# Performance work log

Hardware: AMD Instinct MI355X
Metric: run time of the kernel (lower is better)

The kernel has to match this reference:

```python
import jax, jax.numpy as jnp
import numpy as np

SCALE = 1.0 / np.sqrt(128.0)  # 1/sqrt(head_size)
NEG = -1000000000.0


def setup_inputs() -> dict:
    key = jax.random.key(0)
    k1, k2, k3, k4 = jax.random.split(key, 4)
    B, H, S, D = 2, 16, 2048, 128
    q = jax.random.normal(k1, (B, H, S, D), dtype=jnp.float32)
    k = jax.random.normal(k2, (B, H, S, D), dtype=jnp.float32)
    v = jax.random.normal(k3, (B, H, S, D), dtype=jnp.float32)
    mask = jax.random.randint(k4, (B, S), 0, 2, dtype=jnp.int32)
    return {"q": q, "k": k, "v": v, "mask": mask}


def reference(q, k, v, mask):
    # scores: [B, H, Sq, Sk]
    scores = jnp.einsum("bhqd,bhkd->bhqk", q, k) * SCALE
    m = mask[:, None, None, :]  # [B,1,1,Sk], broadcast over heads and queries
    scores = jnp.where(m == 0, NEG, scores)
    weights = jax.nn.softmax(scores, axis=-1)
    out = jnp.einsum("bhqk,bhkd->bhqd", weights, v)
    return out
```

## Files before the change

### kernel.cpp

```cpp
#include <hip/hip_runtime.h>
#include <hip/hip_bf16.h>

typedef __attribute__((ext_vector_type(8))) short short8;
typedef __attribute__((ext_vector_type(4))) short short4v;
typedef __attribute__((ext_vector_type(4))) float floatx4;

#define NB 2
#define NH 16
#define NBH 32
#define SS 2048
#define DD 128
#define BQ 256
#define BK 32
#define KTILES (SS / BK)
#define SCALE 0.08838834764831845f
#define LOG2E 1.4426950408889634f
#define MAXB 12.0f
#define MASKED_BIAS -100000.0f

#if __has_builtin(__builtin_amdgcn_mfma_f32_16x16x16bf16_1k)
#define MFMA16(a, b, c) __builtin_amdgcn_mfma_f32_16x16x16bf16_1k(a, b, c, 0, 0, 0)
#elif __has_builtin(__builtin_amdgcn_mfma_f32_16x16x16_bf16)
#define MFMA16(a, b, c) __builtin_amdgcn_mfma_f32_16x16x16_bf16(a, b, c, 0, 0, 0)
#else
__device__ __forceinline__ floatx4 mfma16_asm(short4v a, short4v b, floatx4 c) {
  asm volatile("v_mfma_f32_16x16x16_bf16 %0, %1, %2, %0" : "+v"(c) : "v"(a), "v"(b));
  return c;
}
#define MFMA16(a, b, c) mfma16_asm(a, b, c)
#endif

__device__ __forceinline__ short f2bf(float f) {
  union { float f; unsigned u; } x; x.f = f;
  return (short)((x.u + 0x7FFFu + ((x.u >> 16) & 1u)) >> 16);
}

__device__ __forceinline__ short4v pack4(float a, float b, float c, float d) {
  union { __hip_bfloat162 h2[2]; short4v v; } u;
  u.h2[0] = __float22bfloat162_rn(make_float2(a, b));
  u.h2[1] = __float22bfloat162_rn(make_float2(c, d));
  return u.v;
}

__device__ __forceinline__ void gload_lds16(const short* g, short* l) {
  __builtin_amdgcn_global_load_lds(
      (const __attribute__((address_space(1))) void*)(g),
      (__attribute__((address_space(3))) void*)(l), 16, 0, 0);
}

__global__ __launch_bounds__(256) void prep_kernel(const float* __restrict__ k,
                                                   const float* __restrict__ v,
                                                   short* __restrict__ kbf,
                                                   short* __restrict__ vtg) {
  __shared__ short Ts[DD][68];
  const int kb = blockIdx.x, bh = blockIdx.y;
  const int tid = threadIdx.x;
  const size_t base = (size_t)bh * SS * DD + (size_t)(kb * 64) * DD;
  const float* kr = k + base;
  const float* vr = v + base;
  short* kw = kbf + base;
#pragma unroll
  for (int c = 0; c < 8; ++c) {
    int fi = c * 256 + tid;
    float4 a = ((const float4*)kr)[fi];
    short4v o;
    o[0] = f2bf(a.x); o[1] = f2bf(a.y); o[2] = f2bf(a.z); o[3] = f2bf(a.w);
    *(short4v*)(kw + (size_t)fi * 4) = o;
    float4 vv = ((const float4*)vr)[fi];
    int d0 = (fi * 4) & 127, key = (fi * 4) >> 7;
    Ts[d0 + 0][key] = f2bf(vv.x);
    Ts[d0 + 1][key] = f2bf(vv.y);
    Ts[d0 + 2][key] = f2bf(vv.z);
    Ts[d0 + 3][key] = f2bf(vv.w);
  }
  __syncthreads();
#pragma unroll
  for (int s = 0; s < 4; ++s) {
    int d = s * 32 + (tid >> 3);
    int c = tid & 7, kt2 = c >> 2, g = c & 3;
    short4v lo = *(short4v*)&Ts[d][kt2 * 32 + g * 4];
    short4v hi = *(short4v*)&Ts[d][kt2 * 32 + 16 + g * 4];
    short8 o;
#pragma unroll
    for (int r = 0; r < 4; ++r) { o[r] = lo[r]; o[4 + r] = hi[r]; }
    *(short8*)(vtg + ((size_t)(bh * DD + d)) * SS + (kb * 2 + kt2) * 32 + g * 8) = o;
  }
}

__global__ __launch_bounds__(256) void fa_kernel(
    const float* __restrict__ q, const short* __restrict__ kbf,
    const short* __restrict__ vtg, const int* __restrict__ mask,
    float* __restrict__ out) {
  __shared__ __align__(16) short Ks[2][BK * DD];
  __shared__ __align__(16) short Vt[2][DD * BK];

  const int tid = threadIdx.x;
  const int wave = tid >> 6;
  const int lane = tid & 63;
  const int l16 = lane & 15;
  const int quad = lane >> 4;
  const int bh = blockIdx.y;
  const int b = bh >> 4;
  const int q0 = blockIdx.x * BQ;

  const size_t base = (size_t)bh * SS * DD;
  const float* qg = q + base;
  const short* kg = kbf + base;
  const short* vgb = vtg + (size_t)bh * DD * SS;
  const int4* mg4 = (const int4*)(mask + b * SS);
  const float c1 = SCALE * LOG2E, c2 = MAXB * LOG2E;

  short8 qf[4][4];
#pragma unroll
  for (int t = 0; t < 4; ++t) {
    const float* qp = qg + (size_t)(q0 + wave * 64 + t * 16 + l16) * DD;
#pragma unroll
    for (int dc = 0; dc < 4; ++dc) {
      float4 a = *(const float4*)(qp + dc * 32 + quad * 8);
      float4 bb = *(const float4*)(qp + dc * 32 + quad * 8 + 4);
      short8 tt;
      tt[0] = f2bf(a.x); tt[1] = f2bf(a.y); tt[2] = f2bf(a.z); tt[3] = f2bf(a.w);
      tt[4] = f2bf(bb.x); tt[5] = f2bf(bb.y); tt[6] = f2bf(bb.z); tt[7] = f2bf(bb.w);
      qf[t][dc] = tt;
    }
  }

  floatx4 Oacc[4][8];
#pragma unroll
  for (int t = 0; t < 4; ++t)
#pragma unroll
    for (int f = 0; f < 8; ++f) Oacc[t][f] = (floatx4){0.f, 0.f, 0.f, 0.f};
  float l_acc[4] = {0.f, 0.f, 0.f, 0.f};

  const short* kp[2];
  const short* vp[2];
#pragma unroll
  for (int i = 0; i < 2; ++i) {
    int c = wave * 2 + i;
    int krow = c * 4 + (lane >> 4);
    kp[i] = kg + (size_t)krow * DD + (((lane & 15) ^ (krow & 7)) * 8);
    int d = c * 16 + (lane >> 2);
    vp[i] = vgb + (size_t)d * SS + (((lane & 3) ^ ((lane >> 3) & 3)) * 8);
  }

  int koff[2];
#pragma unroll
  for (int nt = 0; nt < 2; ++nt) koff[nt] = (nt * 16 + l16) * DD;
  const int ksw = l16 & 7;
  const int voff = l16 * 32 + ((quad ^ ((l16 >> 1) & 3)) * 8);

#pragma unroll
  for (int i = 0; i < 2; ++i) {
    int c = wave * 2 + i;
    gload_lds16(kp[i], &Ks[0][c * 512]);
    gload_lds16(vp[i], &Vt[0][c * 512]);
    kp[i] += BK * DD;
    vp[i] += BK;
  }

#pragma unroll 2
  for (int kt = 0; kt < KTILES; ++kt) {
    const int cur = kt & 1;
    __syncthreads();
    if (kt + 1 < KTILES) {
#pragma unroll
      for (int i = 0; i < 2; ++i) {
        int c = wave * 2 + i;
        gload_lds16(kp[i], &Ks[cur ^ 1][c * 512]);
        gload_lds16(vp[i], &Vt[cur ^ 1][c * 512]);
        kp[i] += BK * DD;
        vp[i] += BK;
      }
    }
    int4 mm0 = mg4[kt * 8 + quad];
    int4 mm1 = mg4[kt * 8 + 4 + quad];

    floatx4 sacc[4][2];
#pragma unroll
    for (int t = 0; t < 4; ++t)
#pragma unroll
      for (int nt = 0; nt < 2; ++nt) sacc[t][nt] = (floatx4){0.f, 0.f, 0.f, 0.f};
#pragma unroll
    for (int nt = 0; nt < 2; ++nt)
#pragma unroll
      for (int dc = 0; dc < 4; ++dc) {
        short8 kf = *(const short8*)(&Ks[cur][0] + koff[nt] + (((dc * 4 + quad) ^ ksw) * 8));
        sacc[0][nt] = __builtin_amdgcn_mfma_f32_16x16x32_bf16(kf, qf[0][dc], sacc[0][nt], 0, 0, 0);
        sacc[1][nt] = __builtin_amdgcn_mfma_f32_16x16x32_bf16(kf, qf[1][dc], sacc[1][nt], 0, 0, 0);
        sacc[2][nt] = __builtin_amdgcn_mfma_f32_16x16x32_bf16(kf, qf[2][dc], sacc[2][nt], 0, 0, 0);
        sacc[3][nt] = __builtin_amdgcn_mfma_f32_16x16x32_bf16(kf, qf[3][dc], sacc[3][nt], 0, 0, 0);
      }

    float b0[4], b1[4];
    b0[0] = mm0.x ? -c2 : MASKED_BIAS;
    b0[1] = mm0.y ? -c2 : MASKED_BIAS;
    b0[2] = mm0.z ? -c2 : MASKED_BIAS;
    b0[3] = mm0.w ? -c2 : MASKED_BIAS;
    b1[0] = mm1.x ? -c2 : MASKED_BIAS;
    b1[1] = mm1.y ? -c2 : MASKED_BIAS;
    b1[2] = mm1.z ? -c2 : MASKED_BIAS;
    b1[3] = mm1.w ? -c2 : MASKED_BIAS;
    short4v pb[4][2];
#pragma unroll
    for (int t = 0; t < 4; ++t) {
      float e0 = __builtin_amdgcn_exp2f(fmaf(sacc[t][0][0], c1, b0[0]));
      float e1 = __builtin_amdgcn_exp2f(fmaf(sacc[t][0][1], c1, b0[1]));
      float e2 = __builtin_amdgcn_exp2f(fmaf(sacc[t][0][2], c1, b0[2]));
      float e3 = __builtin_amdgcn_exp2f(fmaf(sacc[t][0][3], c1, b0[3]));
      float g0 = __builtin_amdgcn_exp2f(fmaf(sacc[t][1][0], c1, b1[0]));
      float g1 = __builtin_amdgcn_exp2f(fmaf(sacc[t][1][1], c1, b1[1]));
      float g2 = __builtin_amdgcn_exp2f(fmaf(sacc[t][1][2], c1, b1[2]));
      float g3 = __builtin_amdgcn_exp2f(fmaf(sacc[t][1][3], c1, b1[3]));
      l_acc[t] += ((e0 + e1) + (e2 + e3)) + ((g0 + g1) + (g2 + g3));
      pb[t][0] = pack4(e0, e1, e2, e3);
      pb[t][1] = pack4(g0, g1, g2, g3);
    }

#pragma unroll
    for (int f = 0; f < 8; ++f) {
      short8 vv = *(const short8*)(&Vt[cur][0] + f * 512 + voff);
      short4v va0 = __builtin_shufflevector(vv, vv, 0, 1, 2, 3);
      short4v va1 = __builtin_shufflevector(vv, vv, 4, 5, 6, 7);
#pragma unroll
      for (int t = 0; t < 4; ++t) {
        Oacc[t][f] = MFMA16(va0, pb[t][0], Oacc[t][f]);
        Oacc[t][f] = MFMA16(va1, pb[t][1], Oacc[t][f]);
      }
    }
  }

  float* og = out + base;
#pragma unroll
  for (int t = 0; t < 4; ++t) {
    float s = l_acc[t];
    s += __shfl_xor(s, 16);
    s += __shfl_xor(s, 32);
    float inv = 1.0f / s;
    float* orow = og + (size_t)(q0 + wave * 64 + t * 16 + l16) * DD + quad * 4;
#pragma unroll
    for (int f = 0; f < 8; ++f) {
      float4 w;
      w.x = Oacc[t][f][0] * inv;
      w.y = Oacc[t][f][1] * inv;
      w.z = Oacc[t][f][2] * inv;
      w.w = Oacc[t][f][3] * inv;
      *(float4*)(orow + f * 16) = w;
    }
  }
}

extern "C" void kernel_launch(void* const* d_in, const int* in_sizes, int n_in,
                              void* d_out, int out_size, void* d_ws, size_t ws_size,
                              hipStream_t stream) {
  const float* q = (const float*)d_in[0];
  const float* k = (const float*)d_in[1];
  const float* v = (const float*)d_in[2];
  const int* mask = (const int*)d_in[3];
  float* out = (float*)d_out;

  short* kbf = (short*)d_ws;
  short* vtg = kbf + (size_t)NBH * SS * DD;

  prep_kernel<<<dim3(SS / 64, NBH), dim3(256), 0, stream>>>(k, v, kbf, vtg);
  fa_kernel<<<dim3(SS / BQ, NBH), dim3(256), 0, stream>>>(q, kbf, vtg, mask, out);
}
```

Before: 248.1 us.

## Halve query tile and use 16x16x32 MFMA for the PV product

Shrinks the query block from 256 to 128 rows, so each wave handles 32 query rows instead of 64, and requests two blocks per CU through launch bounds. The PV product now packs the probabilities into 8-element bf16 vectors and issues a single 16x16x32 MFMA per tile, replacing pairs of 16x16x16 MFMAs. The goal is to cut register pressure and raise occupancy, double the grid size for better CU fill, and halve the PV MFMA instruction count. In exchange, K/V tiles are loaded into LDS twice as often in total, since each block now covers fewer queries.

```diff
diff --git a/kernel.cpp b/kernel.cpp
--- a/kernel.cpp
+++ b/kernel.cpp
@@ -10,7 +10,7 @@
 #define NBH 32
 #define SS 2048
 #define DD 128
-#define BQ 256
+#define BQ 128
 #define BK 32
 #define KTILES (SS / BK)
 #define SCALE 0.08838834764831845f
@@ -18,28 +18,19 @@
 #define MAXB 12.0f
 #define MASKED_BIAS -100000.0f
 
-#if __has_builtin(__builtin_amdgcn_mfma_f32_16x16x16bf16_1k)
-#define MFMA16(a, b, c) __builtin_amdgcn_mfma_f32_16x16x16bf16_1k(a, b, c, 0, 0, 0)
-#elif __has_builtin(__builtin_amdgcn_mfma_f32_16x16x16_bf16)
-#define MFMA16(a, b, c) __builtin_amdgcn_mfma_f32_16x16x16_bf16(a, b, c, 0, 0, 0)
-#else
-__device__ __forceinline__ floatx4 mfma16_asm(short4v a, short4v b, floatx4 c) {
-  asm volatile("v_mfma_f32_16x16x16_bf16 %0, %1, %2, %0" : "+v"(c) : "v"(a), "v"(b));
-  return c;
-}
-#define MFMA16(a, b, c) mfma16_asm(a, b, c)
-#endif
-
 __device__ __forceinline__ short f2bf(float f) {
   union { float f; unsigned u; } x; x.f = f;
   return (short)((x.u + 0x7FFFu + ((x.u >> 16) & 1u)) >> 16);
 }
 
-__device__ __forceinline__ short4v pack4(float a, float b, float c, float d) {
-  union { __hip_bfloat162 h2[2]; short4v v; } u;
+__device__ __forceinline__ void pack8(short8* dst, float a, float b, float c, float d,
+                                      float e, float f, float g, float h) {
+  union { __hip_bfloat162 h2[4]; short8 v; } u;
   u.h2[0] = __float22bfloat162_rn(make_float2(a, b));
   u.h2[1] = __float22bfloat162_rn(make_float2(c, d));
-  return u.v;
+  u.h2[2] = __float22bfloat162_rn(make_float2(e, f));
+  u.h2[3] = __float22bfloat162_rn(make_float2(g, h));
+  *dst = u.v;
 }
 
 __device__ __forceinline__ void gload_lds16(const short* g, short* l) {
@@ -87,7 +78,7 @@
   }
 }
 
-__global__ __launch_bounds__(256) void fa_kernel(
+__global__ __launch_bounds__(256, 2) void fa_kernel(
     const float* __restrict__ q, const short* __restrict__ kbf,
     const short* __restrict__ vtg, const int* __restrict__ mask,
     float* __restrict__ out) {
@@ -110,10 +101,10 @@
   const int4* mg4 = (const int4*)(mask + b * SS);
   const float c1 = SCALE * LOG2E, c2 = MAXB * LOG2E;
 
-  short8 qf[4][4];
-#pragma unroll
-  for (int t = 0; t < 4; ++t) {
-    const float* qp = qg + (size_t)(q0 + wave * 64 + t * 16 + l16) * DD;
+  short8 qf[2][4];
+#pragma unroll
+  for (int t = 0; t < 2; ++t) {
+    const float* qp = qg + (size_t)(q0 + wave * 32 + t * 16 + l16) * DD;
 #pragma unroll
     for (int dc = 0; dc < 4; ++dc) {
       float4 a = *(const float4*)(qp + dc * 32 + quad * 8);
@@ -125,12 +116,12 @@
     }
   }
 
-  floatx4 Oacc[4][8];
-#pragma unroll
-  for (int t = 0; t < 4; ++t)
+  floatx4 Oacc[2][8];
+#pragma unroll
+  for (int t = 0; t < 2; ++t)
 #pragma unroll
     for (int f = 0; f < 8; ++f) Oacc[t][f] = (floatx4){0.f, 0.f, 0.f, 0.f};
-  float l_acc[4] = {0.f, 0.f, 0.f, 0.f};
+  float l_acc[2] = {0.f, 0.f};
 
   const short* kp[2];
   const short* vp[2];
@@ -175,9 +166,9 @@
     int4 mm0 = mg4[kt * 8 + quad];
     int4 mm1 = mg4[kt * 8 + 4 + quad];
 
-    floatx4 sacc[4][2];
-#pragma unroll
-    for (int t = 0; t < 4; ++t)
+    floatx4 sacc[2][2];
+#pragma unroll
+    for (int t = 0; t < 2; ++t)
 #pragma unroll
       for (int nt = 0; nt < 2; ++nt) sacc[t][nt] = (floatx4){0.f, 0.f, 0.f, 0.f};
 #pragma unroll
@@ -187,8 +178,6 @@
         short8 kf = *(const short8*)(&Ks[cur][0] + koff[nt] + (((dc * 4 + quad) ^ ksw) * 8));
         sacc[0][nt] = __builtin_amdgcn_mfma_f32_16x16x32_bf16(kf, qf[0][dc], sacc[0][nt], 0, 0, 0);
         sacc[1][nt] = __builtin_amdgcn_mfma_f32_16x16x32_bf16(kf, qf[1][dc], sacc[1][nt], 0, 0, 0);
-        sacc[2][nt] = __builtin_amdgcn_mfma_f32_16x16x32_bf16(kf, qf[2][dc], sacc[2][nt], 0, 0, 0);
-        sacc[3][nt] = __builtin_amdgcn_mfma_f32_16x16x32_bf16(kf, qf[3][dc], sacc[3][nt], 0, 0, 0);
       }
 
     float b0[4], b1[4];
@@ -200,9 +189,9 @@
     b1[1] = mm1.y ? -c2 : MASKED_BIAS;
     b1[2] = mm1.z ? -c2 : MASKED_BIAS;
     b1[3] = mm1.w ? -c2 : MASKED_BIAS;
-    short4v pb[4][2];
-#pragma unroll
-    for (int t = 0; t < 4; ++t) {
+    short8 pb[2];
+#pragma unroll
+    for (int t = 0; t < 2; ++t) {
       float e0 = __builtin_amdgcn_exp2f(fmaf(sacc[t][0][0], c1, b0[0]));
       float e1 = __builtin_amdgcn_exp2f(fmaf(sacc[t][0][1], c1, b0[1]));
       float e2 = __builtin_amdgcn_exp2f(fmaf(sacc[t][0][2], c1, b0[2]));
@@ -212,31 +201,25 @@
       float g2 = __builtin_amdgcn_exp2f(fmaf(sacc[t][1][2], c1, b1[2]));
       float g3 = __builtin_amdgcn_exp2f(fmaf(sacc[t][1][3], c1, b1[3]));
       l_acc[t] += ((e0 + e1) + (e2 + e3)) + ((g0 + g1) + (g2 + g3));
-      pb[t][0] = pack4(e0, e1, e2, e3);
-      pb[t][1] = pack4(g0, g1, g2, g3);
+      pack8(&pb[t], e0, e1, e2, e3, g0, g1, g2, g3);
     }
 
 #pragma unroll
     for (int f = 0; f < 8; ++f) {
       short8 vv = *(const short8*)(&Vt[cur][0] + f * 512 + voff);
-      short4v va0 = __builtin_shufflevector(vv, vv, 0, 1, 2, 3);
-      short4v va1 = __builtin_shufflevector(vv, vv, 4, 5, 6, 7);
-#pragma unroll
-      for (int t = 0; t < 4; ++t) {
-        Oacc[t][f] = MFMA16(va0, pb[t][0], Oacc[t][f]);
-        Oacc[t][f] = MFMA16(va1, pb[t][1], Oacc[t][f]);
-      }
+      Oacc[0][f] = __builtin_amdgcn_mfma_f32_16x16x32_bf16(vv, pb[0], Oacc[0][f], 0, 0, 0);
+      Oacc[1][f] = __builtin_amdgcn_mfma_f32_16x16x32_bf16(vv, pb[1], Oacc[1][f], 0, 0, 0);
     }
   }
 
   float* og = out + base;
 #pragma unroll
-  for (int t = 0; t < 4; ++t) {
+  for (int t = 0; t < 2; ++t) {
     float s = l_acc[t];
     s += __shfl_xor(s, 16);
     s += __shfl_xor(s, 32);
     float inv = 1.0f / s;
-    float* orow = og + (size_t)(q0 + wave * 64 + t * 16 + l16) * DD + quad * 4;
+    float* orow = og + (size_t)(q0 + wave * 32 + t * 16 + l16) * DD + quad * 4;
 #pragma unroll
     for (int f = 0; f < 8; ++f) {
       float4 w;
```

New measurement: 218.8 us. -11.8%, faster.
